# Kernel tuning notes

Hardware: AMD Instinct MI355X
Metric: run time of the kernel (lower is better)

## Reference

```python
import jax, jax.numpy as jnp
import numpy as np

D, H, W = 256, 256, 256
R = 6                      # max_radius: per-Gaussian half-window in voxels


def setup_inputs() -> dict:
    key = jax.random.key(0)
    k1, k2, k3, k4, k5 = jax.random.split(key, 5)
    N = 20000
    center_vox = jax.random.uniform(k1, (N, 3), minval=float(R), maxval=float(D - R), dtype=jnp.float32)
    A = jax.random.normal(k2, (N, 3, 3), dtype=jnp.float32) * 0.5
    # SPD inverse covariance in normalized coords (diffs divided by half_shape ~128)
    cov_inv = (jnp.einsum('nij,nkj->nik', A, A) + jnp.eye(3, dtype=jnp.float32)) * 2000.0
    density_r = jax.random.normal(k3, (N,), dtype=jnp.float32)
    density_i = jax.random.normal(k4, (N,), dtype=jnp.float32)
    radius_vox = jax.random.uniform(k5, (N,), minval=3.0, maxval=float(R), dtype=jnp.float32)
    half_shape = jnp.array([D / 2.0, H / 2.0, W / 2.0], dtype=jnp.float32)
    return {
        'center_vox': center_vox,
        'cov_inv': cov_inv,
        'density_r': density_r,
        'density_i': density_i,
        'radius_vox': radius_vox,
        'half_shape': half_shape,
    }


def reference(center_vox, cov_inv, density_r, density_i, radius_vox, half_shape):
    # Per-Gaussian fixed window of side (2R+1); gather -> Mahalanobis weight -> scatter-add.
    offs = jnp.arange(-R, R + 1, dtype=jnp.int32)
    od, oh, ow = jnp.meshgrid(offs, offs, offs, indexing='ij')
    off = jnp.stack([od, oh, ow], axis=-1).reshape(-1, 3)          # [K3,3]
    base = jnp.floor(center_vox).astype(jnp.int32)                  # [N,3]
    vox = base[:, None, :] + off[None, :, :]                        # [N,K3,3] int
    voxf = vox.astype(center_vox.dtype)
    diff = (voxf - center_vox[:, None, :]) / half_shape             # normalized diff [N,K3,3]
    Md = jnp.einsum('nkd,nde,nke->nk', diff, cov_inv, diff)         # Mahalanobis [N,K3]
    # bbox mask (floor(c-r) .. ceil(c+r)) as in build_tile_pairs / CUDA kernel
    bmin = jnp.floor(center_vox - radius_vox[:, None])
    bmax = jnp.ceil(center_vox + radius_vox[:, None])
    in_bbox = jnp.all((voxf >= bmin[:, None, :]) & (voxf <= bmax[:, None, :]), axis=-1)
    dims = jnp.array([D, H, W], dtype=jnp.int32)
    in_grid = jnp.all((vox >= 0) & (vox < dims), axis=-1)
    mask = (Md <= 9.0) & in_bbox & in_grid
    w = jnp.exp(-0.5 * Md) * mask.astype(Md.dtype)                  # [N,K3]
    flat = jnp.where(in_grid, vox[..., 0] * (H * W) + vox[..., 1] * W + vox[..., 2], 0).reshape(-1)
    vol_r = jnp.zeros(D * H * W, dtype=w.dtype).at[flat].add((w * density_r[:, None]).reshape(-1))
    vol_i = jnp.zeros(D * H * W, dtype=w.dtype).at[flat].add((w * density_i[:, None]).reshape(-1))
    return vol_r.reshape(D, H, W), vol_i.reshape(D, H, W)
```

## Files before the change

### kernel.cpp

```cpp
#include <hip/hip_runtime.h>

#define DD 256
#define HH 256
#define WW 256
#define RMAX 6

#define NTILES 65536
#define CAP 24
#define RECSZ 16
#define OVF_CAP 8192

__global__ __launch_bounds__(256) void fill_kernel(
    const float* __restrict__ center, const float* __restrict__ cov_inv,
    const float* __restrict__ dens_r, const float* __restrict__ dens_i,
    const float* __restrict__ radius, const float* __restrict__ half_shape,
    int* __restrict__ tile_cnt, float* __restrict__ tile_recs,
    int* __restrict__ ovf_cnt, int* __restrict__ ovf_list, int N)
{
    int i = blockIdx.x * 256 + threadIdx.x;
    if (i >= N) return;
    float cx = center[3*i+0], cy = center[3*i+1], cz = center[3*i+2];
    float r  = radius[i];
    float c00=cov_inv[9*i+0], c01=cov_inv[9*i+1], c02=cov_inv[9*i+2];
    float c11=cov_inv[9*i+4], c12=cov_inv[9*i+5], c22=cov_inv[9*i+8];

    float d00 = c11*c22 - c12*c12;
    float d11 = c00*c22 - c02*c02;
    float d22 = c00*c11 - c01*c01;
    float det = c00*d00 - c01*(c01*c22 - c02*c12) + c02*(c01*c12 - c02*c11);
    float k9  = 9.0f / det;
    float hx = half_shape[0], hy = half_shape[1], hz = half_shape[2];
    float ex = hx * sqrtf(d00 * k9) * 1.0001f + 0.01f;
    float ey = hy * sqrtf(d11 * k9) * 1.0001f + 0.01f;
    float ez = hz * sqrtf(d22 * k9) * 1.0001f + 0.01f;
    float rx = fminf(r, ex), ry = fminf(r, ey), rz = fminf(r, ez);

    int bx=(int)floorf(cx), by=(int)floorf(cy), bz=(int)floorf(cz);
    int xlo = max(max((int)floorf(cx - rx), bx - RMAX), 0);
    int xhi = min(min((int)ceilf (cx + rx), bx + RMAX), DD - 1);
    int ylo = max(max((int)floorf(cy - ry), by - RMAX), 0);
    int yhi = min(min((int)ceilf (cy + ry), by + RMAX), HH - 1);
    int zlo = max(max((int)floorf(cz - rz), bz - RMAX), 0);
    int zhi = min(min((int)ceilf (cz + rz), bz + RMAX), WW - 1);
    if (xlo > xhi || ylo > yhi || zlo > zhi) return;

    unsigned lo = (unsigned)xlo | ((unsigned)ylo << 8) | ((unsigned)zlo << 16);
    unsigned hi = (unsigned)xhi | ((unsigned)yhi << 8) | ((unsigned)zhi << 16);
    float4 r0 = make_float4(cx, cy, cz, c00);
    float4 r1 = make_float4(c11, c22, c01 + c01, c02 + c02);
    float4 r2 = make_float4(c12 + c12, dens_r[i], dens_i[i], __uint_as_float(lo));
    float4 r3 = make_float4(__uint_as_float(hi), 0.f, 0.f, 0.f);

    for (int tx = xlo >> 2; tx <= (xhi >> 2); ++tx)
        for (int ty = ylo >> 2; ty <= (yhi >> 2); ++ty)
            for (int tz = zlo >> 4; tz <= (zhi >> 4); ++tz) {
                int tile = (tx << 10) | (ty << 4) | tz;
                int pos = atomicAdd(&tile_cnt[tile], 1);
                if (pos < CAP) {
                    float4* R = (float4*)(tile_recs + ((size_t)tile * CAP + pos) * RECSZ);
                    R[0] = r0; R[1] = r1; R[2] = r2; R[3] = r3;
                } else {
                    int o = atomicAdd(ovf_cnt, 1);
                    if (o < OVF_CAP) { ovf_list[2*o] = tile; ovf_list[2*o+1] = i; }
                }
            }
}

__global__ __launch_bounds__(256) void gather_kernel(
    const int* __restrict__ tile_cnt, const float* __restrict__ tile_recs,
    const float* __restrict__ half_shape,
    float* __restrict__ vol_r, float* __restrict__ vol_i)
{
    __shared__ float4 lds[4 * CAP * 4];
    int w = threadIdx.x >> 6, lane = threadIdx.x & 63;
    int tile = (blockIdx.x << 2) | w;
    int tz = tile & 15, ty = (tile >> 4) & 63, tx = tile >> 10;
    int dxl = lane >> 4, dyl = (lane >> 2) & 3, dzq = lane & 3;
    int vx = tx*4 + dxl, vy = ty*4 + dyl, vz0 = tz*16 + dzq*4;
    float vxf = (float)vx, vyf = (float)vy, vz0f = (float)vz0;
    float ihx = 1.0f/half_shape[0], ihy = 1.0f/half_shape[1], ihz = 1.0f/half_shape[2];

    int n = min(tile_cnt[tile], CAP);
    float4* wl = lds + w * (CAP * 4);
    const float4* src = (const float4*)(tile_recs + (size_t)tile * CAP * RECSZ);
    for (int idx = lane; idx < n * 4; idx += 64) wl[idx] = src[idx];
    __syncthreads();

    float ar0=0.f, ar1=0.f, ar2=0.f, ar3=0.f;
    float ai0=0.f, ai1=0.f, ai2=0.f, ai3=0.f;

    for (int j = 0; j < n; ++j) {
        float4 r0 = wl[j*4+0];
        float4 r1 = wl[j*4+1];
        float4 r2 = wl[j*4+2];
        float4 r3 = wl[j*4+3];
        float cx=r0.x, cy=r0.y, cz=r0.z, s00=r0.w;
        float s11=r1.x, s22=r1.y, s01=r1.z, s02=r1.w;
        float s12=r2.x, dr=r2.y, di=r2.z;
        unsigned lo = __float_as_uint(r2.w), hi = __float_as_uint(r3.x);
        int xlo = lo & 255, ylo = (lo >> 8) & 255, zlo = (lo >> 16) & 255;
        int xhi = hi & 255, yhi = (hi >> 8) & 255, zhi = (hi >> 16) & 255;

        bool okxy = (vx >= xlo) & (vx <= xhi) & (vy >= ylo) & (vy <= yhi);
        float fx = (vxf - cx) * ihx;
        float fy = (vyf - cy) * ihy;
        float axy = fx*fx*s00 + fx*fy*s01 + fy*fy*s11;
        float bxy = fx*s02 + fy*s12;
        float nczihz = -cz * ihz;

        float fz0 = fmaf(vz0f, ihz, nczihz);
        float fz1 = fz0 + ihz;
        float fz2 = fz1 + ihz;
        float fz3 = fz2 + ihz;
        float md0 = fmaf(fz0, fmaf(s22, fz0, bxy), axy);
        float md1 = fmaf(fz1, fmaf(s22, fz1, bxy), axy);
        float md2 = fmaf(fz2, fmaf(s22, fz2, bxy), axy);
        float md3 = fmaf(fz3, fmaf(s22, fz3, bxy), axy);

        bool ok0 = okxy & (vz0   >= zlo) & (vz0   <= zhi) & (md0 <= 9.0f);
        bool ok1 = okxy & (vz0+1 >= zlo) & (vz0+1 <= zhi) & (md1 <= 9.0f);
        bool ok2 = okxy & (vz0+2 >= zlo) & (vz0+2 <= zhi) & (md2 <= 9.0f);
        bool ok3 = okxy & (vz0+3 >= zlo) & (vz0+3 <= zhi) & (md3 <= 9.0f);

        if (__any(ok0 | ok1 | ok2 | ok3)) {
            float w0 = ok0 ? __expf(md0 * -0.5f) : 0.0f;
            float w1 = ok1 ? __expf(md1 * -0.5f) : 0.0f;
            float w2 = ok2 ? __expf(md2 * -0.5f) : 0.0f;
            float w3 = ok3 ? __expf(md3 * -0.5f) : 0.0f;
            ar0 = fmaf(w0, dr, ar0); ai0 = fmaf(w0, di, ai0);
            ar1 = fmaf(w1, dr, ar1); ai1 = fmaf(w1, di, ai1);
            ar2 = fmaf(w2, dr, ar2); ai2 = fmaf(w2, di, ai2);
            ar3 = fmaf(w3, dr, ar3); ai3 = fmaf(w3, di, ai3);
        }
    }

    size_t flat = ((size_t)vx * HH + vy) * WW + vz0;
    *(float4*)(vol_r + flat) = make_float4(ar0, ar1, ar2, ar3);
    *(float4*)(vol_i + flat) = make_float4(ai0, ai1, ai2, ai3);
}

__global__ __launch_bounds__(64) void ovf_kernel(
    const int* __restrict__ ovf_cnt, const int* __restrict__ ovf_list,
    const float* __restrict__ center, const float* __restrict__ cov_inv,
    const float* __restrict__ dens_r, const float* __restrict__ dens_i,
    const float* __restrict__ radius, const float* __restrict__ half_shape,
    float* __restrict__ vol_r, float* __restrict__ vol_i)
{
    int total = min(ovf_cnt[0], OVF_CAP);
    float ihx = 1.0f/half_shape[0], ihy = 1.0f/half_shape[1], ihz = 1.0f/half_shape[2];
    int lane = threadIdx.x;
    for (int p = blockIdx.x; p < total; p += gridDim.x) {
        int tile = ovf_list[2*p], g = ovf_list[2*p+1];
        int tz = tile & 15, ty = (tile >> 4) & 63, tx = tile >> 10;
        int dxl = lane >> 4, dyl = (lane >> 2) & 3, dzq = lane & 3;
        int vx = tx*4 + dxl, vy = ty*4 + dyl, vz0 = tz*16 + dzq*4;

        float cx = center[3*g+0], cy = center[3*g+1], cz = center[3*g+2];
        float r  = radius[g];
        float c00=cov_inv[9*g+0], c01=cov_inv[9*g+1], c02=cov_inv[9*g+2];
        float c10=cov_inv[9*g+3], c11=cov_inv[9*g+4], c12=cov_inv[9*g+5];
        float c20=cov_inv[9*g+6], c21=cov_inv[9*g+7], c22=cov_inv[9*g+8];
        float dr = dens_r[g], di = dens_i[g];

        int bx=(int)floorf(cx), by=(int)floorf(cy), bz=(int)floorf(cz);
        int xlo = max(max((int)floorf(cx - r), bx - RMAX), 0);
        int xhi = min(min((int)ceilf (cx + r), bx + RMAX), DD - 1);
        int ylo = max(max((int)floorf(cy - r), by - RMAX), 0);
        int yhi = min(min((int)ceilf (cy + r), by + RMAX), HH - 1);
        int zlo = max(max((int)floorf(cz - r), bz - RMAX), 0);
        int zhi = min(min((int)ceilf (cz + r), bz + RMAX), WW - 1);

        if (vx < xlo || vx > xhi || vy < ylo || vy > yhi) continue;
        float fx = ((float)vx - cx) * ihx;
        float fy = ((float)vy - cy) * ihy;
        for (int k = 0; k < 4; ++k) {
            int vz = vz0 + k;
            float fz = ((float)vz - cz) * ihz;
            float md = fx*(c00*fx + c01*fy + c02*fz)
                     + fy*(c10*fx + c11*fy + c12*fz)
                     + fz*(c20*fx + c21*fy + c22*fz);
            if (vz >= zlo && vz <= zhi && md <= 9.0f) {
                float wgt = __expf(-0.5f * md);
                size_t flat = ((size_t)vx * HH + vy) * WW + vz;
                atomicAdd(&vol_r[flat], wgt * dr);
                atomicAdd(&vol_i[flat], wgt * di);
            }
        }
    }
}

__global__ __launch_bounds__(256) void splat_kernel(
    const float* __restrict__ center, const float* __restrict__ cov_inv,
    const float* __restrict__ dens_r, const float* __restrict__ dens_i,
    const float* __restrict__ radius, const float* __restrict__ half_shape,
    float* __restrict__ vol_r, float* __restrict__ vol_i, int N)
{
    int g = blockIdx.x;
    if (g >= N) return;
    float cx = center[3*g+0], cy = center[3*g+1], cz = center[3*g+2];
    float r  = radius[g];
    float c00 = cov_inv[9*g+0], c01 = cov_inv[9*g+1], c02 = cov_inv[9*g+2];
    float c10 = cov_inv[9*g+3], c11 = cov_inv[9*g+4], c12 = cov_inv[9*g+5];
    float c20 = cov_inv[9*g+6], c21 = cov_inv[9*g+7], c22 = cov_inv[9*g+8];
    float dr = dens_r[g], di = dens_i[g];
    float ihx = 1.0f/half_shape[0], ihy = 1.0f/half_shape[1], ihz = 1.0f/half_shape[2];
    int bx = (int)floorf(cx), by = (int)floorf(cy), bz = (int)floorf(cz);
    int xlo = max(max((int)floorf(cx - r), bx - RMAX), 0);
    int xhi = min(min((int)ceilf (cx + r), bx + RMAX), DD - 1);
    int ylo = max(max((int)floorf(cy - r), by - RMAX), 0);
    int yhi = min(min((int)ceilf (cy + r), by + RMAX), HH - 1);
    int zlo = max(max((int)floorf(cz - r), bz - RMAX), 0);
    int zhi = min(min((int)ceilf (cz + r), bz + RMAX), WW - 1);
    int nx = xhi-xlo+1, ny = yhi-ylo+1, nz = zhi-zlo+1;
    if (nx <= 0 || ny <= 0 || nz <= 0) return;
    int total = nx*ny*nz;
    for (int k = threadIdx.x; k < total; k += 256) {
        int iz = k % nz, tq = k / nz, iy = tq % ny, ix = tq / ny;
        int vx = xlo+ix, vy = ylo+iy, vz = zlo+iz;
        float dxn = ((float)vx - cx) * ihx;
        float dyn = ((float)vy - cy) * ihy;
        float dzn = ((float)vz - cz) * ihz;
        float md = dxn*(c00*dxn + c01*dyn + c02*dzn)
                 + dyn*(c10*dxn + c11*dyn + c12*dzn)
                 + dzn*(c20*dxn + c21*dyn + c22*dzn);
        if (md <= 9.0f) {
            float wgt = __expf(-0.5f*md);
            int flat = (vx*HH + vy)*WW + vz;
            atomicAdd(&vol_r[flat], wgt*dr);
            atomicAdd(&vol_i[flat], wgt*di);
        }
    }
}

extern "C" void kernel_launch(void* const* d_in, const int* in_sizes, int n_in,
                              void* d_out, int out_size, void* d_ws, size_t ws_size,
                              hipStream_t stream) {
    const float* center     = (const float*)d_in[0];
    const float* cov_inv    = (const float*)d_in[1];
    const float* dens_r     = (const float*)d_in[2];
    const float* dens_i     = (const float*)d_in[3];
    const float* radius     = (const float*)d_in[4];
    const float* half_shape = (const float*)d_in[5];
    int N = in_sizes[0] / 3;

    float* vol_r = (float*)d_out;
    float* vol_i = vol_r + (size_t)DD * HH * WW;

    size_t rec_floats = (size_t)NTILES * CAP * RECSZ;
    size_t need = rec_floats * sizeof(float)
                + ((size_t)NTILES + 4 + 2*OVF_CAP) * sizeof(int);
    if (ws_size < need) {
        (void)hipMemsetAsync(d_out, 0, (size_t)out_size * sizeof(float), stream);
        splat_kernel<<<N, 256, 0, stream>>>(center, cov_inv, dens_r, dens_i,
                                            radius, half_shape, vol_r, vol_i, N);
        return;
    }

    float* tile_recs = (float*)d_ws;
    int*   tile_cnt  = (int*)(tile_recs + rec_floats);
    int*   ovf_cnt   = tile_cnt + NTILES;
    int*   ovf_list  = ovf_cnt + 4;

    (void)hipMemsetAsync(tile_cnt, 0, ((size_t)NTILES + 4) * sizeof(int), stream);
    fill_kernel<<<(N + 255)/256, 256, 0, stream>>>(center, cov_inv, dens_r, dens_i,
                                                   radius, half_shape,
                                                   tile_cnt, tile_recs,
                                                   ovf_cnt, ovf_list, N);
    gather_kernel<<<NTILES/4, 256, 0, stream>>>(tile_cnt, tile_recs, half_shape,
                                                vol_r, vol_i);
    ovf_kernel<<<64, 64, 0, stream>>>(ovf_cnt, ovf_list, center, cov_inv,
                                      dens_r, dens_i, radius, half_shape,
                                      vol_r, vol_i);
}
```

Baseline: 219.7 us.

## Parallelise tile binning across a wavefront per Gaussian and trim gather checks

The fill kernel now assigns one 64-lane wavefront per Gaussian, with each lane handling one overlapped tile, instead of one thread looping serially over all tiles. This targets the serialised atomics and record writes in binning, at the cost of redundant per-lane setup math and idle lanes. The gather kernel drops a block-wide barrier, since each wave only uses its own shared slice, and replaces paired bbox comparisons with unsigned range checks.

```diff
diff --git a/kernel.cpp b/kernel.cpp
--- a/kernel.cpp
+++ b/kernel.cpp
@@ -17,8 +17,10 @@
     int* __restrict__ tile_cnt, float* __restrict__ tile_recs,
     int* __restrict__ ovf_cnt, int* __restrict__ ovf_list, int N)
 {
-    int i = blockIdx.x * 256 + threadIdx.x;
+    int lane = threadIdx.x & 63;
+    int i = __builtin_amdgcn_readfirstlane(blockIdx.x * 4 + (threadIdx.x >> 6));
     if (i >= N) return;
+
     float cx = center[3*i+0], cy = center[3*i+1], cz = center[3*i+2];
     float r  = radius[i];
     float c00=cov_inv[9*i+0], c01=cov_inv[9*i+1], c02=cov_inv[9*i+2];
@@ -44,6 +46,13 @@
     int zhi = min(min((int)ceilf (cz + rz), bz + RMAX), WW - 1);
     if (xlo > xhi || ylo > yhi || zlo > zhi) return;
 
+    int tx0 = xlo >> 2, ntx = (xhi >> 2) - tx0 + 1;
+    int ty0 = ylo >> 2, nty = (yhi >> 2) - ty0 + 1;
+    int tz0 = zlo >> 4, ntz = (zhi >> 4) - tz0 + 1;
+    int ntiles = ntx * nty * ntz;
+
+    if (lane >= ntiles) return;
+
     unsigned lo = (unsigned)xlo | ((unsigned)ylo << 8) | ((unsigned)zlo << 16);
     unsigned hi = (unsigned)xhi | ((unsigned)yhi << 8) | ((unsigned)zhi << 16);
     float4 r0 = make_float4(cx, cy, cz, c00);
@@ -51,19 +60,20 @@
     float4 r2 = make_float4(c12 + c12, dens_r[i], dens_i[i], __uint_as_float(lo));
     float4 r3 = make_float4(__uint_as_float(hi), 0.f, 0.f, 0.f);
 
-    for (int tx = xlo >> 2; tx <= (xhi >> 2); ++tx)
-        for (int ty = ylo >> 2; ty <= (yhi >> 2); ++ty)
-            for (int tz = zlo >> 4; tz <= (zhi >> 4); ++tz) {
-                int tile = (tx << 10) | (ty << 4) | tz;
-                int pos = atomicAdd(&tile_cnt[tile], 1);
-                if (pos < CAP) {
-                    float4* R = (float4*)(tile_recs + ((size_t)tile * CAP + pos) * RECSZ);
-                    R[0] = r0; R[1] = r1; R[2] = r2; R[3] = r3;
-                } else {
-                    int o = atomicAdd(ovf_cnt, 1);
-                    if (o < OVF_CAP) { ovf_list[2*o] = tile; ovf_list[2*o+1] = i; }
-                }
-            }
+    int t = lane;
+    int tzz = tz0 + (t % ntz); t /= ntz;
+    int tyy = ty0 + (t % nty); t /= nty;
+    int txx = tx0 + t;
+    int tile = (txx << 10) | (tyy << 4) | tzz;
+
+    int pos = atomicAdd(&tile_cnt[tile], 1);
+    if (pos < CAP) {
+        float4* R = (float4*)(tile_recs + ((size_t)tile * CAP + pos) * RECSZ);
+        R[0] = r0; R[1] = r1; R[2] = r2; R[3] = r3;
+    } else {
+        int o = atomicAdd(ovf_cnt, 1);
+        if (o < OVF_CAP) { ovf_list[2*o] = tile; ovf_list[2*o+1] = i; }
+    }
 }
 
 __global__ __launch_bounds__(256) void gather_kernel(
@@ -84,7 +94,6 @@
     float4* wl = lds + w * (CAP * 4);
     const float4* src = (const float4*)(tile_recs + (size_t)tile * CAP * RECSZ);
     for (int idx = lane; idx < n * 4; idx += 64) wl[idx] = src[idx];
-    __syncthreads();
 
     float ar0=0.f, ar1=0.f, ar2=0.f, ar3=0.f;
     float ai0=0.f, ai1=0.f, ai2=0.f, ai3=0.f;
@@ -101,7 +110,11 @@
         int xlo = lo & 255, ylo = (lo >> 8) & 255, zlo = (lo >> 16) & 255;
         int xhi = hi & 255, yhi = (hi >> 8) & 255, zhi = (hi >> 16) & 255;
 
-        bool okxy = (vx >= xlo) & (vx <= xhi) & (vy >= ylo) & (vy <= yhi);
+        bool okxy = ((unsigned)(vx - xlo) <= (unsigned)(xhi - xlo)) &
+                    ((unsigned)(vy - ylo) <= (unsigned)(yhi - ylo));
+        int iz0 = vz0 - zlo;
+        unsigned zspan = (unsigned)(zhi - zlo);
+
         float fx = (vxf - cx) * ihx;
         float fy = (vyf - cy) * ihy;
         float axy = fx*fx*s00 + fx*fy*s01 + fy*fy*s11;
@@ -117,10 +130,10 @@
         float md2 = fmaf(fz2, fmaf(s22, fz2, bxy), axy);
         float md3 = fmaf(fz3, fmaf(s22, fz3, bxy), axy);
 
-        bool ok0 = okxy & (vz0   >= zlo) & (vz0   <= zhi) & (md0 <= 9.0f);
-        bool ok1 = okxy & (vz0+1 >= zlo) & (vz0+1 <= zhi) & (md1 <= 9.0f);
-        bool ok2 = okxy & (vz0+2 >= zlo) & (vz0+2 <= zhi) & (md2 <= 9.0f);
-        bool ok3 = okxy & (vz0+3 >= zlo) & (vz0+3 <= zhi) & (md3 <= 9.0f);
+        bool ok0 = okxy & ((unsigned)(iz0    ) <= zspan) & (md0 <= 9.0f);
+        bool ok1 = okxy & ((unsigned)(iz0 + 1) <= zspan) & (md1 <= 9.0f);
+        bool ok2 = okxy & ((unsigned)(iz0 + 2) <= zspan) & (md2 <= 9.0f);
+        bool ok3 = okxy & ((unsigned)(iz0 + 3) <= zspan) & (md3 <= 9.0f);
 
         if (__any(ok0 | ok1 | ok2 | ok3)) {
             float w0 = ok0 ? __expf(md0 * -0.5f) : 0.0f;
@@ -262,10 +275,10 @@
     int*   ovf_list  = ovf_cnt + 4;
 
     (void)hipMemsetAsync(tile_cnt, 0, ((size_t)NTILES + 4) * sizeof(int), stream);
-    fill_kernel<<<(N + 255)/256, 256, 0, stream>>>(center, cov_inv, dens_r, dens_i,
-                                                   radius, half_shape,
-                                                   tile_cnt, tile_recs,
-                                                   ovf_cnt, ovf_list, N);
+    fill_kernel<<<(N + 3)/4, 256, 0, stream>>>(center, cov_inv, dens_r, dens_i,
+                                               radius, half_shape,
+                                               tile_cnt, tile_recs,
+                                               ovf_cnt, ovf_list, N);
     gather_kernel<<<NTILES/4, 256, 0, stream>>>(tile_cnt, tile_recs, half_shape,
                                                 vol_r, vol_i);
     ovf_kernel<<<64, 64, 0, stream>>>(ovf_cnt, ovf_list, center, cov_inv,
```

After: 200.4 us. -8.8%, faster.
